# Performance work log

Measured on AMD Instinct MI355X. Metric: run time of the kernel, lower is better.

Reference implementation:

```python
import jax, jax.numpy as jnp
import numpy as np

B, N, C, D = 64, 1024, 128, 64

def setup_inputs() -> dict:
    key = jax.random.key(0)
    ks = jax.random.split(key, 7)
    # kaiming_normal_ on weights (fan_in = C), default zero-ish biases kept as Linear default uniform; use small uniform
    std = float(np.sqrt(2.0 / C))
    bb = float(1.0 / np.sqrt(C))
    return {
        "x": jax.random.normal(ks[0], (B, N, C), jnp.float32),
        "Wq": jax.random.normal(ks[1], (C, D), jnp.float32) * std,
        "bq": jax.random.uniform(ks[2], (D,), jnp.float32, -bb, bb),
        "Wk": jax.random.normal(ks[3], (C, D), jnp.float32) * std,
        "bk": jax.random.uniform(ks[4], (D,), jnp.float32, -bb, bb),
        "Wv": jax.random.normal(ks[5], (C, D), jnp.float32) * std,
        "bv": jax.random.uniform(ks[6], (D,), jnp.float32, -bb, bb),
    }

def reference(x, Wq, bq, Wk, bk, Wv, bv):
    q = jax.nn.relu(jnp.einsum('bnc,cd->bnd', x, Wq) + bq)  # [B,N,D]
    k = jax.nn.relu(jnp.einsum('bnc,cd->bnd', x, Wk) + bk)
    v = jax.nn.relu(jnp.einsum('bnc,cd->bnd', x, Wv) + bv)
    scores = jnp.einsum('bnd,bmd->bnm', q, k) / jnp.sqrt(jnp.asarray(D, q.dtype))
    attn = jax.nn.softmax(scores, axis=-1)
    out = jnp.einsum('bnm,bmd->bnd', attn, v)
    return out + q
```

## Files before the change

kernel.cpp:

```cpp
#include <hip/hip_runtime.h>
#include <hip/hip_bf16.h>


#define Bsz 64
#define Nsz 1024
#define Csz 128
#define Dsz 64

typedef __attribute__((ext_vector_type(8))) short short8;
typedef __attribute__((ext_vector_type(4))) float f32x4;

__device__ __forceinline__ unsigned short f2bf(float f) {
    union { float f; unsigned u; } v; v.f = f;
    unsigned r = v.u + 0x7FFF + ((v.u >> 16) & 1);
    return (unsigned short)(r >> 16);
}
__device__ __forceinline__ float bf2f(unsigned short h) {
    union { unsigned u; float f; } v; v.u = ((unsigned)h) << 16;
    return v.f;
}
__device__ __forceinline__ unsigned pack_bf16rn(float lo, float hi) {
    unsigned ulo = __float_as_uint(lo) + 0x8000u;
    unsigned uhi = __float_as_uint(hi) + 0x8000u;
    return __builtin_amdgcn_perm(uhi, ulo, 0x07060302u);
}

#define SCq (0.125f * 1.44269504f)
#define INV_SC (1.0f / (0.125f * 1.44269504f))

__global__ __launch_bounds__(256) void wprep_kernel(
    const float* __restrict__ Wq, const float* __restrict__ Wk,
    const float* __restrict__ Wv, unsigned short* __restrict__ wfrag)
{
    int t = blockIdx.x * 256 + threadIdx.x;
    int lane = t & 63, ksi = (t >> 6) & 3, dt = t >> 8;
    int l16 = lane & 15, quad = lane >> 4;
    int d = dt * 16 + l16;
    int c0 = ksi * 32 + quad * 8;
    short8 q8, k8, v8;
    #pragma unroll
    for (int j = 0; j < 8; j++) {
        q8[j] = (short)f2bf(Wq[(c0 + j) * Dsz + d]);
        k8[j] = (short)f2bf(Wk[(c0 + j) * Dsz + d]);
        v8[j] = (short)f2bf(Wv[(c0 + j) * Dsz + d]);
    }
    int idx = (dt * 4 + ksi) * 64 + lane;
    ((short8*)wfrag)[0 * 1024 + idx] = q8;
    ((short8*)wfrag)[1 * 1024 + idx] = k8;
    ((short8*)wfrag)[2 * 1024 + idx] = v8;
}

__global__ __launch_bounds__(256) void qkv_kernel(
    const float* __restrict__ x, const unsigned short* __restrict__ wfrag,
    const float* __restrict__ bq, const float* __restrict__ bk,
    const float* __restrict__ bv,
    unsigned short* __restrict__ qs, unsigned short* __restrict__ ks2,
    unsigned short* __restrict__ vt2)
{
    __shared__ short lds[16384];
    short* xh = lds;
    const int t    = threadIdx.x;
    const int lane = t & 63;
    const int l16  = lane & 15, quad = lane >> 4;
    const int dt   = t >> 6;
    const long rowbase = (long)blockIdx.x * 64;
    const int d = dt * 16 + l16;

    short8 wqf[4], wkf[4], wvf[4];
    #pragma unroll
    for (int ksi = 0; ksi < 4; ksi++) {
        int idx = (dt * 4 + ksi) * 64 + lane;
        wqf[ksi] = ((const short8*)wfrag)[0 * 1024 + idx];
        wkf[ksi] = ((const short8*)wfrag)[1 * 1024 + idx];
        wvf[ksi] = ((const short8*)wfrag)[2 * 1024 + idx];
    }

    {
        const int row = t & 63;
        const float* xrow = x + (rowbase + row) * Csz;
        #pragma unroll
        for (int p = 0; p < 4; p++) {
            int cb = (t >> 6) + p * 4;
            float4 a  = *(const float4*)(xrow + cb * 8);
            float4 bb = *(const float4*)(xrow + cb * 8 + 4);
            uint4 hi4;
            hi4.x = pack_bf16rn(a.x,  a.y);
            hi4.y = pack_bf16rn(a.z,  a.w);
            hi4.z = pack_bf16rn(bb.x, bb.y);
            hi4.w = pack_bf16rn(bb.z, bb.w);
            int unit = ((row >> 4) * 4 + (cb >> 2)) * 64 + ((row & 15) | ((cb & 3) << 4));
            *(uint4*)&xh[unit * 8] = hi4;
        }
    }
    __syncthreads();

    f32x4 aq[4], ak[4], av[4];
    #pragma unroll
    for (int i = 0; i < 4; i++) {
        aq[i] = (f32x4){0.f, 0.f, 0.f, 0.f};
        ak[i] = (f32x4){0.f, 0.f, 0.f, 0.f};
        av[i] = (f32x4){0.f, 0.f, 0.f, 0.f};
    }
    #pragma unroll
    for (int ksi = 0; ksi < 4; ksi++) {
        #pragma unroll
        for (int rt = 0; rt < 4; rt++) {
            short8 ah = *(const short8*)&xh[((rt * 4 + ksi) * 64 + lane) * 8];
            aq[rt] = __builtin_amdgcn_mfma_f32_16x16x32_bf16(ah, wqf[ksi], aq[rt], 0, 0, 0);
            ak[rt] = __builtin_amdgcn_mfma_f32_16x16x32_bf16(ah, wkf[ksi], ak[rt], 0, 0, 0);
            av[rt] = __builtin_amdgcn_mfma_f32_16x16x32_bf16(ah, wvf[ksi], av[rt], 0, 0, 0);
        }
    }

    const float bqd = bq[d], bkd = bk[d], bvd = bv[d];
    const long b  = rowbase >> 10;
    const int  kt = (int)((rowbase >> 6) & 15);

    __syncthreads();
    short* stq = lds;
    short* stk = lds + 4608;
    short* stv = lds + 9216;

    float vv[4][4];
    #pragma unroll
    for (int rt = 0; rt < 4; rt++) {
        #pragma unroll
        for (int r = 0; r < 4; r++) {
            int nl = rt * 16 + quad * 4 + r;
            float q = fmaxf(aq[rt][r] + bqd, 0.f);
            float k = fmaxf(ak[rt][r] + bkd, 0.f);
            vv[r][rt] = fmaxf(av[rt][r] + bvd, 0.f);
            stq[nl * 72 + d] = (short)f2bf(q * SCq);
            stk[nl * 72 + d] = (short)f2bf(k);
        }
    }
    #pragma unroll
    for (int r = 0; r < 4; r++) {
        int slot = (dt * 2 + (quad >> 1)) * 64 + (((quad & 1) << 1) | (r >> 1)) * 16 + l16;
        uint2 pk = make_uint2(pack_bf16rn(vv[r][0], vv[r][1]),
                              pack_bf16rn(vv[r][2], vv[r][3]));
        *(uint2*)&stv[slot * 8 + (r & 1) * 4] = pk;
    }
    __syncthreads();

    const long tbase = (long)(b * 16 + kt) * 512;
    #pragma unroll
    for (int i = 0; i < 2; i++) {
        int sidx = i * 256 + t;
        int row = sidx >> 3, g = sidx & 7;
        short8 vq = *(const short8*)&stq[row * 72 + g * 8];
        ((short8*)qs)[(rowbase + row) * 8 + g] = vq;
        int kb = sidx >> 7, rem = sidx & 127, half = rem >> 6, lam = rem & 63;
        short8 vk = *(const short8*)&stk[(kb * 16 + (lam & 15)) * 72 + half * 32 + (lam >> 4) * 8];
        ((short8*)ks2)[tbase + kb * 128 + half * 64 + lam] = vk;
        short8 v8 = *(const short8*)&stv[sidx * 8];
        ((short8*)vt2)[tbase + sidx] = v8;
    }
}

__global__ __launch_bounds__(256) void attn_kernel(
    const unsigned short* __restrict__ qs,
    const unsigned short* __restrict__ ks2,
    const unsigned short* __restrict__ vt2,
    float* __restrict__ out)
{
    __shared__ short Pl[4][32][72];

    const int t    = threadIdx.x;
    const int wave = t >> 6;
    const int lane = t & 63;
    const int l16  = lane & 15;
    const int quad = lane >> 4;
    const int b    = blockIdx.x & 63;
    const int qh   = blockIdx.x >> 6;
    const int qbase = qh * 128 + wave * 32;

    const short8* ks8 = (const short8*)ks2 + (long)b * 8192;
    const short8* vt8 = (const short8*)vt2 + (long)b * 8192;

    short8 aq[2][2];
    #pragma unroll
    for (int s = 0; s < 2; s++) {
        const unsigned short* qp = qs + ((long)b * Nsz + qbase + s * 16 + l16) * Dsz + quad * 8;
        aq[s][0] = *(const short8*)(qp);
        aq[s][1] = *(const short8*)(qp + 32);
    }

    f32x4 O[2][4];
    float lsum[2][4];
    #pragma unroll
    for (int s = 0; s < 2; s++)
        #pragma unroll
        for (int i = 0; i < 4; i++) { O[s][i] = (f32x4){0.f,0.f,0.f,0.f}; lsum[s][i] = 0.f; }

    short8 kfA[4][2], kfB[4][2];
    #pragma unroll
    for (int kb = 0; kb < 4; kb++) {
        kfA[kb][0] = ks8[(kb * 2 + 0) * 64 + lane];
        kfA[kb][1] = ks8[(kb * 2 + 1) * 64 + lane];
    }

    auto step = [&](int kt, short8 (&cur)[4][2], short8 (&nxt)[4][2]) {
        short8 bvf[2][4];
        #pragma unroll
        for (int cb = 0; cb < 4; cb++) {
            bvf[0][cb] = vt8[((long)kt * 8 + cb * 2 + 0) * 64 + lane];
            bvf[1][cb] = vt8[((long)kt * 8 + cb * 2 + 1) * 64 + lane];
        }

        f32x4 sc[2][4];
        #pragma unroll
        for (int s = 0; s < 2; s++) {
            #pragma unroll
            for (int kb = 0; kb < 4; kb++) {
                f32x4 z = (f32x4){0.f, 0.f, 0.f, 0.f};
                z = __builtin_amdgcn_mfma_f32_16x16x32_bf16(aq[s][0], cur[kb][0], z, 0, 0, 0);
                z = __builtin_amdgcn_mfma_f32_16x16x32_bf16(aq[s][1], cur[kb][1], z, 0, 0, 0);
                sc[s][kb] = z;
            }
        }

        {
            int ktn = (kt + 1) & 15;
            #pragma unroll
            for (int kb = 0; kb < 4; kb++) {
                nxt[kb][0] = ks8[((long)ktn * 8 + kb * 2 + 0) * 64 + lane];
                nxt[kb][1] = ks8[((long)ktn * 8 + kb * 2 + 1) * 64 + lane];
            }
        }

        #pragma unroll
        for (int s = 0; s < 2; s++) {
            #pragma unroll
            for (int r = 0; r < 4; r++) {
                float p0 = __builtin_amdgcn_exp2f(sc[s][0][r]);
                float p1 = __builtin_amdgcn_exp2f(sc[s][1][r]);
                float p2 = __builtin_amdgcn_exp2f(sc[s][2][r]);
                float p3 = __builtin_amdgcn_exp2f(sc[s][3][r]);
                lsum[s][r] += (p0 + p1) + (p2 + p3);
                *(uint2*)&Pl[wave][s * 16 + quad * 4 + r][l16 * 4] =
                    make_uint2(pack_bf16rn(p0, p1), pack_bf16rn(p2, p3));
            }
        }

        #pragma unroll
        for (int ck = 0; ck < 2; ck++) {
            #pragma unroll
            for (int s = 0; s < 2; s++) {
                short8 ap = *(const short8*)&Pl[wave][s * 16 + l16][ck * 32 + quad * 8];
                #pragma unroll
                for (int cb = 0; cb < 4; cb++) {
                    O[s][cb] = __builtin_amdgcn_mfma_f32_16x16x32_bf16(ap, bvf[ck][cb], O[s][cb], 0, 0, 0);
                }
            }
        }
    };

    for (int kt = 0; kt < 16; kt += 2) {
        step(kt,     kfA, kfB);
        step(kt + 1, kfB, kfA);
    }

    #pragma unroll
    for (int s = 0; s < 2; s++)
        #pragma unroll
        for (int r = 0; r < 4; r++)
            #pragma unroll
            for (int off = 1; off < 16; off <<= 1)
                lsum[s][r] += __shfl_xor(lsum[s][r], off);

    float* fst = (float*)&Pl[wave][0][0];
    #pragma unroll
    for (int s = 0; s < 2; s++) {
        #pragma unroll
        for (int r = 0; r < 4; r++) {
            float rl = 1.0f / lsum[s][r];
            #pragma unroll
            for (int cb = 0; cb < 4; cb++)
                fst[(quad * 4 + r) * 68 + cb * 16 + l16] = O[s][cb][r] * rl;
        }
        #pragma unroll
        for (int j = 0; j < 4; j++) {
            int vidx = j * 64 + lane;
            int row = vidx >> 4, dp = (vidx & 15) * 4;
            f32x4 ov = *(const f32x4*)&fst[row * 68 + dp];
            long nrow = (long)b * Nsz + qbase + s * 16 + row;
            uint2 qv = *(const uint2*)(qs + nrow * Dsz + dp);
            ov[0] += bf2f((unsigned short)(qv.x)) * INV_SC;
            ov[1] += bf2f((unsigned short)(qv.x >> 16)) * INV_SC;
            ov[2] += bf2f((unsigned short)(qv.y)) * INV_SC;
            ov[3] += bf2f((unsigned short)(qv.y >> 16)) * INV_SC;
            *(f32x4*)(out + nrow * Dsz + dp) = ov;
        }
    }
}

extern "C" void kernel_launch(void* const* d_in, const int* in_sizes, int n_in,
                              void* d_out, int out_size, void* d_ws, size_t ws_size,
                              hipStream_t stream) {
    const float* x  = (const float*)d_in[0];
    const float* Wq = (const float*)d_in[1];
    const float* bq = (const float*)d_in[2];
    const float* Wk = (const float*)d_in[3];
    const float* bk = (const float*)d_in[4];
    const float* Wv = (const float*)d_in[5];
    const float* bv = (const float*)d_in[6];
    float* out = (float*)d_out;

    char* ws = (char*)d_ws;
    unsigned short* qsc   = (unsigned short*)ws;
    unsigned short* ks2   = (unsigned short*)(ws + 0x1000000);
    unsigned short* vt2   = (unsigned short*)(ws + 0x2000000);
    unsigned short* wfrag = (unsigned short*)(ws + 0x3000000);

    wprep_kernel<<<dim3(4), dim3(256), 0, stream>>>(Wq, Wk, Wv, wfrag);
    qkv_kernel<<<dim3(1024), dim3(256), 0, stream>>>(
        x, wfrag, bq, bk, bv, qsc, ks2, vt2);
    attn_kernel<<<dim3(512), dim3(256), 0, stream>>>(
        qsc, ks2, vt2, out);
}
```

Before: 124.5 us.

## Compute transposed scores so P feeds PV MFMA from registers, dropping LDS

Swaps the operands of the QK^T MFMA so the score accumulator comes out transposed. In that layout each lane's four exp'd probabilities are already a valid bf16 operand for a 16x16x16 MFMA, so P no longer goes through an LDS round-trip. The V tile is re-laid out in the projection kernel to match the new 16x16x16 operand format, and the epilogue writes output directly from accumulators with a simpler row-sum reduction. The cost is twice as many, smaller MFMA instructions for the PV product.

```diff
diff --git a/kernel.cpp b/kernel.cpp
--- a/kernel.cpp
+++ b/kernel.cpp
@@ -8,6 +8,7 @@
 #define Dsz 64
 
 typedef __attribute__((ext_vector_type(8))) short short8;
+typedef __attribute__((ext_vector_type(4))) short short4v;
 typedef __attribute__((ext_vector_type(4))) float f32x4;
 
 __device__ __forceinline__ unsigned short f2bf(float f) {
@@ -23,6 +24,15 @@
     unsigned ulo = __float_as_uint(lo) + 0x8000u;
     unsigned uhi = __float_as_uint(hi) + 0x8000u;
     return __builtin_amdgcn_perm(uhi, ulo, 0x07060302u);
+}
+__device__ __forceinline__ f32x4 mfma_16x16x16_bf16(short4v a, short4v b, f32x4 c) {
+#if __has_builtin(__builtin_amdgcn_mfma_f32_16x16x16bf16_1k)
+    return __builtin_amdgcn_mfma_f32_16x16x16bf16_1k(a, b, c, 0, 0, 0);
+#else
+    asm volatile("v_mfma_f32_16x16x16_bf16 %0, %1, %2, %0"
+                 : "+v"(c) : "v"(a), "v"(b));
+    return c;
+#endif
 }
 
 #define SCq (0.125f * 1.44269504f)
@@ -135,11 +145,10 @@
         }
     }
     #pragma unroll
-    for (int r = 0; r < 4; r++) {
-        int slot = (dt * 2 + (quad >> 1)) * 64 + (((quad & 1) << 1) | (r >> 1)) * 16 + l16;
-        uint2 pk = make_uint2(pack_bf16rn(vv[r][0], vv[r][1]),
-                              pack_bf16rn(vv[r][2], vv[r][3]));
-        *(uint2*)&stv[slot * 8 + (r & 1) * 4] = pk;
+    for (int rt = 0; rt < 4; rt++) {
+        uint2 pk = make_uint2(pack_bf16rn(vv[0][rt], vv[1][rt]),
+                              pack_bf16rn(vv[2][rt], vv[3][rt]));
+        *(uint2*)&stv[((rt * 4 + dt) * 64 + lane) * 4] = pk;
     }
     __syncthreads();
 
@@ -153,8 +162,7 @@
         int kb = sidx >> 7, rem = sidx & 127, half = rem >> 6, lam = rem & 63;
         short8 vk = *(const short8*)&stk[(kb * 16 + (lam & 15)) * 72 + half * 32 + (lam >> 4) * 8];
         ((short8*)ks2)[tbase + kb * 128 + half * 64 + lam] = vk;
-        short8 v8 = *(const short8*)&stv[sidx * 8];
-        ((short8*)vt2)[tbase + sidx] = v8;
+        ((uint4*)vt2)[tbase + sidx] = *(const uint4*)&stv[sidx * 8];
     }
 }
 
@@ -164,8 +172,6 @@
     const unsigned short* __restrict__ vt2,
     float* __restrict__ out)
 {
-    __shared__ short Pl[4][32][72];
-
     const int t    = threadIdx.x;
     const int wave = t >> 6;
     const int lane = t & 63;
@@ -176,7 +182,7 @@
     const int qbase = qh * 128 + wave * 32;
 
     const short8* ks8 = (const short8*)ks2 + (long)b * 8192;
-    const short8* vt8 = (const short8*)vt2 + (long)b * 8192;
+    const uint2*  vt8 = (const uint2*)vt2 + (long)b * 16384;
 
     short8 aq[2][2];
     #pragma unroll
@@ -187,11 +193,11 @@
     }
 
     f32x4 O[2][4];
-    float lsum[2][4];
+    float lsum[2] = {0.f, 0.f};
     #pragma unroll
     for (int s = 0; s < 2; s++)
         #pragma unroll
-        for (int i = 0; i < 4; i++) { O[s][i] = (f32x4){0.f,0.f,0.f,0.f}; lsum[s][i] = 0.f; }
+        for (int i = 0; i < 4; i++) O[s][i] = (f32x4){0.f, 0.f, 0.f, 0.f};
 
     short8 kfA[4][2], kfB[4][2];
     #pragma unroll
@@ -201,12 +207,12 @@
     }
 
     auto step = [&](int kt, short8 (&cur)[4][2], short8 (&nxt)[4][2]) {
-        short8 bvf[2][4];
-        #pragma unroll
-        for (int cb = 0; cb < 4; cb++) {
-            bvf[0][cb] = vt8[((long)kt * 8 + cb * 2 + 0) * 64 + lane];
-            bvf[1][cb] = vt8[((long)kt * 8 + cb * 2 + 1) * 64 + lane];
-        }
+        uint2 vr[4][4];
+        #pragma unroll
+        for (int kb = 0; kb < 4; kb++)
+            #pragma unroll
+            for (int cb = 0; cb < 4; cb++)
+                vr[kb][cb] = vt8[(long)kt * 1024 + (kb * 4 + cb) * 64 + lane];
 
         f32x4 sc[2][4];
         #pragma unroll
@@ -214,8 +220,8 @@
             #pragma unroll
             for (int kb = 0; kb < 4; kb++) {
                 f32x4 z = (f32x4){0.f, 0.f, 0.f, 0.f};
-                z = __builtin_amdgcn_mfma_f32_16x16x32_bf16(aq[s][0], cur[kb][0], z, 0, 0, 0);
-                z = __builtin_amdgcn_mfma_f32_16x16x32_bf16(aq[s][1], cur[kb][1], z, 0, 0, 0);
+                z = __builtin_amdgcn_mfma_f32_16x16x32_bf16(cur[kb][0], aq[s][0], z, 0, 0, 0);
+                z = __builtin_amdgcn_mfma_f32_16x16x32_bf16(cur[kb][1], aq[s][1], z, 0, 0, 0);
                 sc[s][kb] = z;
             }
         }
@@ -232,25 +238,18 @@
         #pragma unroll
         for (int s = 0; s < 2; s++) {
             #pragma unroll
-            for (int r = 0; r < 4; r++) {
-                float p0 = __builtin_amdgcn_exp2f(sc[s][0][r]);
-                float p1 = __builtin_amdgcn_exp2f(sc[s][1][r]);
-                float p2 = __builtin_amdgcn_exp2f(sc[s][2][r]);
-                float p3 = __builtin_amdgcn_exp2f(sc[s][3][r]);
-                lsum[s][r] += (p0 + p1) + (p2 + p3);
-                *(uint2*)&Pl[wave][s * 16 + quad * 4 + r][l16 * 4] =
-                    make_uint2(pack_bf16rn(p0, p1), pack_bf16rn(p2, p3));
-            }
-        }
-
-        #pragma unroll
-        for (int ck = 0; ck < 2; ck++) {
-            #pragma unroll
-            for (int s = 0; s < 2; s++) {
-                short8 ap = *(const short8*)&Pl[wave][s * 16 + l16][ck * 32 + quad * 8];
+            for (int kb = 0; kb < 4; kb++) {
+                float p0 = __builtin_amdgcn_exp2f(sc[s][kb][0]);
+                float p1 = __builtin_amdgcn_exp2f(sc[s][kb][1]);
+                float p2 = __builtin_amdgcn_exp2f(sc[s][kb][2]);
+                float p3 = __builtin_amdgcn_exp2f(sc[s][kb][3]);
+                lsum[s] += (p0 + p1) + (p2 + p3);
+                union { uint2 u; short4v s4; } bp;
+                bp.u = make_uint2(pack_bf16rn(p0, p1), pack_bf16rn(p2, p3));
                 #pragma unroll
                 for (int cb = 0; cb < 4; cb++) {
-                    O[s][cb] = __builtin_amdgcn_mfma_f32_16x16x32_bf16(ap, bvf[ck][cb], O[s][cb], 0, 0, 0);
+                    union { uint2 u; short4v s4; } va; va.u = vr[kb][cb];
+                    O[s][cb] = mfma_16x16x16_bf16(va.s4, bp.s4, O[s][cb]);
                 }
             }
         }
@@ -262,35 +261,25 @@
     }
 
     #pragma unroll
-    for (int s = 0; s < 2; s++)
-        #pragma unroll
-        for (int r = 0; r < 4; r++)
-            #pragma unroll
-            for (int off = 1; off < 16; off <<= 1)
-                lsum[s][r] += __shfl_xor(lsum[s][r], off);
-
-    float* fst = (float*)&Pl[wave][0][0];
-    #pragma unroll
     for (int s = 0; s < 2; s++) {
-        #pragma unroll
-        for (int r = 0; r < 4; r++) {
-            float rl = 1.0f / lsum[s][r];
-            #pragma unroll
-            for (int cb = 0; cb < 4; cb++)
-                fst[(quad * 4 + r) * 68 + cb * 16 + l16] = O[s][cb][r] * rl;
-        }
-        #pragma unroll
-        for (int j = 0; j < 4; j++) {
-            int vidx = j * 64 + lane;
-            int row = vidx >> 4, dp = (vidx & 15) * 4;
-            f32x4 ov = *(const f32x4*)&fst[row * 68 + dp];
-            long nrow = (long)b * Nsz + qbase + s * 16 + row;
-            uint2 qv = *(const uint2*)(qs + nrow * Dsz + dp);
-            ov[0] += bf2f((unsigned short)(qv.x)) * INV_SC;
-            ov[1] += bf2f((unsigned short)(qv.x >> 16)) * INV_SC;
-            ov[2] += bf2f((unsigned short)(qv.y)) * INV_SC;
-            ov[3] += bf2f((unsigned short)(qv.y >> 16)) * INV_SC;
-            *(f32x4*)(out + nrow * Dsz + dp) = ov;
+        lsum[s] += __shfl_xor(lsum[s], 16);
+        lsum[s] += __shfl_xor(lsum[s], 32);
+    }
+
+    #pragma unroll
+    for (int s = 0; s < 2; s++) {
+        float rl = 1.0f / lsum[s];
+        long nrow = (long)b * Nsz + qbase + s * 16 + l16;
+        #pragma unroll
+        for (int cb = 0; cb < 4; cb++) {
+            int d0 = cb * 16 + quad * 4;
+            uint2 qv = *(const uint2*)(qs + nrow * Dsz + d0);
+            f32x4 ov;
+            ov[0] = O[s][cb][0] * rl + bf2f((unsigned short)(qv.x)) * INV_SC;
+            ov[1] = O[s][cb][1] * rl + bf2f((unsigned short)(qv.x >> 16)) * INV_SC;
+            ov[2] = O[s][cb][2] * rl + bf2f((unsigned short)(qv.y)) * INV_SC;
+            ov[3] = O[s][cb][3] * rl + bf2f((unsigned short)(qv.y >> 16)) * INV_SC;
+            *(f32x4*)(out + nrow * Dsz + d0) = ov;
         }
     }
 }
```

New measurement: 135.2 us. +8.6%, slower.
